# Kernel optimization log

Hardware: AMD Instinct MI355X
Metric: run time of the kernel (lower is better)

The kernel has to match this reference:

```python
import jax, jax.numpy as jnp
import numpy as np

B, T, D = 128, 150, 100
NQ, NS, NU = 50000, 2000, 20000
QNB, SNB, UNB, Q2NB = 4, 10, 10, 5
HOPS, RANK_K = 3, 10
NEG = -1e9


def _linear(x, W, b):
    return x @ W.T + b


def _aggregate(hops, agg_W, agg_b, last_W, last_b):
    # triangular multi-hop mean-aggregate, mirrors sqgkt.aggregate (dropout in eval mode)
    hops = list(hops)
    n = len(hops) - 1
    for i in range(n):
        for j in range(n - i):
            s = jnp.mean(hops[j + 1], axis=-2) + hops[j]
            hops[j] = jax.nn.relu(_linear(s, agg_W[j], agg_b[j]))
    return jax.nn.relu(_linear(hops[0], last_W, last_b))


def forward_impl(floats, ints):
    (emb_q, emb_q2, emb_s, emb_u, emb_r, w1_q, w2_q, lin_W, lin_b,
     Wih, Whh, bih, bhh, agg_W, agg_b, last_W, last_b,
     qW, qb, kW, kb, wW, wb, h0, c0) = floats
    (user, question, response, mask, q_neighbors, s_neighbors,
     u_neighbors, q_neighbors_2, qs_skill_ids) = ints

    jpos = jnp.arange(T)
    # detached question embeddings over the full sequence (recap scoring uses .detach())
    eq_sg = jax.lax.stop_gradient(emb_q)[question]  # [B,T,D]
    xs = (user.T[:-1], question.T[:-1], response.T[:-1], (mask == 1).T[:-1],
          question.T[1:], jnp.moveaxis(eq_sg, 1, 0)[1:], jnp.arange(T - 1))

    def predict(qs_concat, hist, hmask):
        # bilinear scores between question/skill embs and history states,
        # attention weights from MLP_W(cat(MLP_query(q), MLP_key(s)))
        g = jnp.einsum('bqd,bsd->bqs', qs_concat, hist)
        sq = _linear(qs_concat, qW, qb) @ wW[0, :D]   # [B,nq]
        sk = _linear(hist, kW, kb) @ wW[0, D:]        # [B,ns]
        score = sq[:, :, None] + sk[:, None, :] + wb[0]
        score = jnp.where(hmask[:, None, :], score, NEG)
        alpha = jax.nn.softmax(score.reshape(B, -1), axis=1)
        return jax.nn.sigmoid(jnp.sum(alpha * g.reshape(B, -1), axis=1))

    def step(carry, x):
        h, c, hist_state = carry
        u_t, q_t, r_t, m_t, q_next, eqn_sg, t = x
        # ---- question/skill multi-hop gather + aggregate (mask selects rows) ----
        n1 = q_neighbors[q_t]              # [B,QNB] skill ids
        n2 = s_neighbors[n1]               # [B,QNB,SNB] question ids
        n3 = q_neighbors[n2]               # [B,QNB,SNB,QNB] skill ids
        agg1 = _aggregate([emb_q[q_t], emb_s[n1], emb_q[n2], emb_s[n3]],
                          agg_W, agg_b, last_W, last_b)
        e_q = jnp.where(m_t[:, None], agg1, emb_q[q_t])
        # ---- user/question multi-hop gather + aggregate ----
        m1 = u_neighbors[u_t]              # [B,UNB] question ids
        m2 = q_neighbors_2[m1]             # [B,UNB,Q2NB] user ids
        m3 = u_neighbors[m2]               # [B,UNB,Q2NB,UNB] question ids
        agg2 = _aggregate([emb_u[u_t], emb_q2[m1], emb_u[m2], emb_q2[m3]],
                          agg_W, agg_b, last_W, last_b)
        e_q2 = jnp.where(m_t[:, None], agg2, emb_q2[q_t])
        emb_hat = w1_q * e_q + w2_q * e_q2
        # ---- LSTM step (torch LSTMCell gate order i,f,g,o) ----
        x_in = jax.nn.relu(_linear(jnp.concatenate([emb_hat, emb_r[r_t]], axis=1), lin_W, lin_b))
        gates = x_in @ Wih.T + bih + h @ Whh.T + bhh
        ig, fg, gg, og = jnp.split(gates, 4, axis=1)
        c = jax.nn.sigmoid(fg) * c + jax.nn.sigmoid(ig) * jnp.tanh(gg)
        h = jax.nn.sigmoid(og) * jnp.tanh(c)
        # ---- next-question + its related skills (fixed QNB skills/question) ----
        qs_concat = jnp.concatenate([emb_q[q_next][:, None], emb_s[qs_skill_ids[q_next]]], axis=1)
        # ---- soft recap: top-k past states by detached emb similarity ----
        scores = jnp.where(jpos[None, :] < t,
                           jnp.einsum('bjd,bd->bj', eq_sg, eqn_sg), -jnp.inf)
        top_vals, top_idx = jax.lax.top_k(scores, RANK_K)
        valid = jnp.isfinite(top_vals)     # fewer than K valid when t<=K
        sel = jnp.where(valid[:, :, None],
                        jnp.take_along_axis(hist_state, top_idx[:, :, None], axis=1), 0.0)
        hist = jnp.concatenate([h[:, None], sel], axis=1)      # [B,K+1,D]
        hmask = jnp.concatenate([jnp.ones((B, 1), bool), valid], axis=1)
        y = predict(qs_concat, hist, hmask)
        # torch skips the state_history write at t==0 (continue), so keep zeros there
        hist_state = hist_state.at[:, t].set(jnp.where(t > 0, h, 0.0))
        return (h, c, hist_state), y

    _, ys = jax.lax.scan(step, (h0, c0, jnp.zeros((B, T, D), jnp.float32)), xs)
    return jnp.concatenate([jnp.full((B, 1), 0.5, jnp.float32), ys.T], axis=1)


def setup_inputs():
    ks = jax.random.split(jax.random.key(0), 40)
    g = lambda i, shape, s=0.05: jax.random.normal(ks[i], shape, dtype=jnp.float32) * s
    ri = lambda i, shape, hi: jax.random.randint(ks[i], shape, 0, hi, dtype=jnp.int32)
    xav = float(np.sqrt(6.0 / (B + D)))  # xavier_uniform_ on a [B,D] zeros tensor
    return {
        'emb_q': g(0, (NQ, D)), 'emb_q2': g(1, (NQ, D)),
        'emb_s': g(2, (NS, D)), 'emb_u': g(3, (NU, D)),
        'emb_r': g(4, (2, D)),
        'w1_q': jnp.float32(0.5), 'w2_q': jnp.float32(0.5),
        'lin_W': g(5, (2 * D, 2 * D)), 'lin_b': jnp.zeros((2 * D,), jnp.float32),
        'Wih': g(6, (4 * D, 2 * D)), 'Whh': g(7, (4 * D, D)),
        'bih': jnp.zeros((4 * D,), jnp.float32), 'bhh': jnp.zeros((4 * D,), jnp.float32),
        'agg_W': g(8, (HOPS, D, D)), 'agg_b': jnp.zeros((HOPS, D), jnp.float32),
        'last_W': g(9, (D, D)), 'last_b': jnp.zeros((D,), jnp.float32),
        'qW': g(10, (D, D)), 'qb': jnp.zeros((D,), jnp.float32),
        'kW': g(11, (D, D)), 'kb': jnp.zeros((D,), jnp.float32),
        'wW': g(12, (1, 2 * D)), 'wb': jnp.zeros((1,), jnp.float32),
        'h0': jax.random.uniform(ks[13], (B, D), jnp.float32, -xav, xav),
        'c0': jax.random.uniform(ks[14], (B, D), jnp.float32, -xav, xav),
        'user': ri(15, (B, T), NU), 'question': ri(16, (B, T), NQ),
        'response': ri(17, (B, T), 2), 'mask': ri(18, (B, T), 2),
        'q_neighbors': ri(19, (NQ, QNB), NS), 's_neighbors': ri(20, (NS, SNB), NQ),
        'u_neighbors': ri(21, (NU, UNB), NQ), 'q_neighbors_2': ri(22, (NQ, Q2NB), NU),
        'qs_skill_ids': ri(23, (NQ, QNB), NS),
    }


def reference(emb_q, emb_q2, emb_s, emb_u, emb_r, w1_q, w2_q, lin_W, lin_b, Wih, Whh, bih, bhh, agg_W, agg_b, last_W, last_b, qW, qb, kW, kb, wW, wb, h0, c0, user, question, response, mask, q_neighbors, s_neighbors, u_neighbors, q_neighbors_2, qs_skill_ids):
    floats = (emb_q, emb_q2, emb_s, emb_u, emb_r, w1_q, w2_q, lin_W, lin_b,
              Wih, Whh, bih, bhh, agg_W, agg_b, last_W, last_b,
              qW, qb, kW, kb, wW, wb, h0, c0)
    ints = (user, question, response, mask, q_neighbors, s_neighbors,
            u_neighbors, q_neighbors_2, qs_skill_ids)
    return forward_impl(floats, ints)
```

## Files before the change

### kernel.cpp

```cpp
#include <hip/hip_runtime.h>
#include <hip/hip_bf16.h>

#define BB 128
#define TT 150
#define TS 149
#define NITEM (TS*BB)

typedef __attribute__((ext_vector_type(8))) short bf16x8;
typedef __attribute__((ext_vector_type(4))) float f32x4;

__device__ __forceinline__ float bf(__hip_bfloat16 x) { return __bfloat162float(x); }
__device__ __forceinline__ __hip_bfloat16 tobf(float x) { return __float2bfloat16(x); }
__device__ __forceinline__ float sigm(float x) { return 1.f / (1.f + expf(-x)); }

__device__ __forceinline__ unsigned pk2(float a, float b) {
  unsigned ua = __float_as_uint(a), ub = __float_as_uint(b);
  ua += 0x7fffu + ((ua >> 16) & 1u);
  ub += 0x7fffu + ((ub >> 16) & 1u);
  return (ua >> 16) | (ub & 0xffff0000u);
}
__device__ __forceinline__ float blo(unsigned u) { return __uint_as_float(u << 16); }
__device__ __forceinline__ float bhi(unsigned u) { return __uint_as_float(u & 0xffff0000u); }

#define PREP_N 3267131
__global__ __launch_bounds__(256, 4) void k_prep(
    const float* __restrict__ agg_W, const float* __restrict__ last_W,
    const float* __restrict__ lin_W, const float* __restrict__ Wih,
    const float* __restrict__ emb_q, const float* __restrict__ emb_q2,
    const float* __restrict__ emb_s, const float* __restrict__ emb_u,
    const int* __restrict__ q_nb, const int* __restrict__ s_nb,
    const int* __restrict__ u_nb, const int* __restrict__ q_nb2,
    const float* __restrict__ Whh,
    const float* __restrict__ qW, const float* __restrict__ qb,
    const float* __restrict__ kW, const float* __restrict__ kb,
    const float* __restrict__ wW, const float* __restrict__ wb,
    __hip_bfloat16* __restrict__ Wb, uint2* __restrict__ W0g, uint2* __restrict__ WLg,
    __hip_bfloat16* __restrict__ linB, __hip_bfloat16* __restrict__ wihB,
    uint2* __restrict__ gQ, uint2* __restrict__ gU,
    uint2* __restrict__ gT1Q, uint2* __restrict__ gT1U,
    uint4* __restrict__ WhP, float* __restrict__ kvqv,
    uint2* __restrict__ W0c, uint2* __restrict__ WLc)
{
  for (int v = blockIdx.x*256 + threadIdx.x; v < PREP_N; v += gridDim.x*256) {
    if (v < 65536) {
      int m = v >> 14, r = v & 16383, c = r >> 7, k = r & 127;
      const float* src = (m==0) ? agg_W+20000 : (m==1) ? agg_W+10000 : (m==2) ? agg_W : last_W;
      Wb[v] = tobf((c < 100 && k < 100) ? src[c*100+k] : 0.f);
    } else if (v < 70536) {
      int j = v - 65536; int mtx = j / 2500; j %= 2500;
      int k4 = j / 100, c = j % 100;
      const float* src = mtx ? last_W : agg_W;
      float4 a = *(const float4*)&src[c*100 + k4*4];
      (mtx ? WLg : W0g)[j] = make_uint2(pk2(a.x,a.y), pk2(a.z,a.w));
    } else if (v < 117128) {
      int j = v - 70536;
      int c = j / 224, k = j % 224;
      linB[j] = tobf((c < 200 && k < 200) ? lin_W[c*200+k] : 0.f);
    } else if (v < 206728) {
      int j = v - 117128;
      int c = j / 224, k = j % 224;
      wihB[j] = tobf((k < 200) ? Wih[c*200+k] : 0.f);
    } else if (v < 1456728) {
      int j = v - 206728, q = j / 25, k4 = j % 25;
      float sx=0.f,sy=0.f,sz=0.f,sw=0.f;
#pragma unroll
      for (int i = 0; i < 4; i++) {
        float4 e = *(const float4*)&emb_s[q_nb[q*4+i]*100 + k4*4];
        sx+=e.x; sy+=e.y; sz+=e.z; sw+=e.w;
      }
      float4 a = *(const float4*)&emb_q[q*100 + k4*4];
      gQ[j] = make_uint2(pk2(0.25f*sx+a.x, 0.25f*sy+a.y), pk2(0.25f*sz+a.z, 0.25f*sw+a.w));
    } else if (v < 1956728) {
      int j = v - 1456728, u = j / 25, k4 = j % 25;
      float sx=0.f,sy=0.f,sz=0.f,sw=0.f;
      for (int k = 0; k < 10; k++) {
        float4 e = *(const float4*)&emb_q2[u_nb[u*10+k]*100 + k4*4];
        sx+=e.x; sy+=e.y; sz+=e.z; sw+=e.w;
      }
      float4 a = *(const float4*)&emb_u[u*100 + k4*4];
      gU[j] = make_uint2(pk2(0.1f*sx+a.x, 0.1f*sy+a.y), pk2(0.1f*sz+a.z, 0.1f*sw+a.w));
    } else if (v < 2006728) {
      int j = v - 1956728, s = j / 25, k4 = j % 25;
      float sx=0.f,sy=0.f,sz=0.f,sw=0.f;
      for (int jj = 0; jj < 10; jj++) {
        float4 e = *(const float4*)&emb_q[s_nb[s*10+jj]*100 + k4*4];
        sx+=e.x; sy+=e.y; sz+=e.z; sw+=e.w;
      }
      float4 a = *(const float4*)&emb_s[s*100 + k4*4];
      gT1Q[j] = make_uint2(pk2(0.1f*sx+a.x, 0.1f*sy+a.y), pk2(0.1f*sz+a.z, 0.1f*sw+a.w));
    } else if (v < 3256728) {
      int j = v - 2006728, q = j / 25, k4 = j % 25;
      float sx=0.f,sy=0.f,sz=0.f,sw=0.f;
#pragma unroll
      for (int p = 0; p < 5; p++) {
        float4 e = *(const float4*)&emb_u[q_nb2[q*5+p]*100 + k4*4];
        sx+=e.x; sy+=e.y; sz+=e.z; sw+=e.w;
      }
      float4 a = *(const float4*)&emb_q2[q*100 + k4*4];
      gT1U[j] = make_uint2(pk2(0.2f*sx+a.x, 0.2f*sy+a.y), pk2(0.2f*sz+a.z, 0.2f*sw+a.w));
    } else if (v < 3261928) {
      int j = v - 3256728; int row = j / 13, k8 = j % 13;
      float vv[8];
#pragma unroll
      for (int r = 0; r < 8; r++) { int k = k8*8 + r; vv[r] = (k < 100) ? Whh[row*100 + k] : 0.f; }
      WhP[j] = make_uint4(pk2(vv[0],vv[1]), pk2(vv[2],vv[3]), pk2(vv[4],vv[5]), pk2(vv[6],vv[7]));
    } else if (v < 3262131) {
      int idx = v - 3261928;
      float s = 0.f;
      if (idx < 100)      { for (int c = 0; c < 100; c++) s += kW[c*100+idx] * wW[100+c]; kvqv[idx] = s; }
      else if (idx < 200) { int t2 = idx-100; for (int c = 0; c < 100; c++) s += qW[c*100+t2] * wW[c]; kvqv[idx] = s; }
      else if (idx == 200){ for (int c = 0; c < 100; c++) s += kb[c] * wW[100+c]; kvqv[200] = s; }
      else if (idx == 201){ for (int c = 0; c < 100; c++) s += qb[c] * wW[c]; kvqv[201] = s; }
      else kvqv[202] = wb[0];
    } else {
      int j = v - 3262131; int mtx = j / 2500; j %= 2500;
      int c = j / 25, k4 = j % 25;
      const float* src = mtx ? last_W : agg_W;
      float4 a = *(const float4*)&src[c*100 + k4*4];
      (mtx ? WLc : W0c)[j] = make_uint2(pk2(a.x,a.y), pk2(a.z,a.w));
    }
  }
}

__global__ __launch_bounds__(512, 6) void k_embhat(
    const float* __restrict__ emb_q, const float* __restrict__ emb_q2,
    const float* __restrict__ w1_q, const float* __restrict__ w2_q,
    const float* __restrict__ agg_b, const float* __restrict__ last_b,
    const int* __restrict__ user, const int* __restrict__ question, const int* __restrict__ mask,
    const int* __restrict__ q_nb, const int* __restrict__ s_nb,
    const int* __restrict__ u_nb, const int* __restrict__ q_nb2,
    const __hip_bfloat16* __restrict__ Wb,
    const uint2* __restrict__ W0c, const uint2* __restrict__ WLc,
    const uint2* __restrict__ gQ, const uint2* __restrict__ gU,
    const uint2* __restrict__ gT1Q, const uint2* __restrict__ gT1U,
    __hip_bfloat16* __restrict__ embhat)
{
  __shared__ __align__(16) char Ab[114*256];
  __shared__ __hip_bfloat16 Cb[114*100];
  __shared__ int n2[40], m2[50], n1[4], m1[10];
  float* S = (float*)Ab;
  const int tid = threadIdx.x, wid = tid >> 6, lane = tid & 63;
  const int l15 = lane & 15, lg = lane >> 4;
  const int item = blockIdx.x;
  const int t = item / BB, b = item % BB;
  const int qt = question[b*TT + t];
  const float w1 = w1_q[0], w2 = w2_q[0];

  if (mask[b*TT + t] != 1) {
    if (tid < 50) {
      const float2 q = *(const float2*)&emb_q[qt*100 + tid*2];
      const float2 p = *(const float2*)&emb_q2[qt*100 + tid*2];
      ((unsigned*)embhat)[item*50 + tid] = pk2(w1*q.x + w2*p.x, w1*q.y + w2*p.y);
    }
    return;
  }
  const int ut = user[b*TT + t];

  bf16x8 w2f[4];
  if (wid < 7) {
#pragma unroll
    for (int kc = 0; kc < 4; kc++)
      w2f[kc] = *(const bf16x8*)(Wb + (wid*16 + l15)*128 + kc*32 + lg*8);
  }

  for (int v = tid; v < 1102; v += 512) {
    if (v < 40) { int n1a = q_nb[qt*4 + v/10]; n2[v] = s_nb[n1a*10 + v%10]; }
    else if (v < 90) { int e = v-40; int m1a = u_nb[ut*10 + e/5]; m2[e] = q_nb2[m1a*5 + e%5]; }
    else if (v < 94) { n1[v-90] = q_nb[qt*4 + (v-90)]; }
    else if (v < 104) { m1[v-94] = u_nb[ut*10 + (v-94)]; }
    else {
      int z = v - 104, row, k4;
      if (z < 798) { row = z/7; k4 = 25 + z%7; }
      else if (z < 948) { int e = z-798; row = 90 + e/25; k4 = e%25; }
      else { int e = z-948; row = 110 + e/25; k4 = e%25; }
      int ofs = (row*256 + k4*8) ^ ((row&7)<<4);
// ... 109 lines not shown
      }
      int col = nt*16 + l15, r0 = mt*16 + lg*4;
      if (col < 100) {
#pragma unroll
        for (int r = 0; r < 4; r++)
          if (r0 + r < 114) Cb[(r0+r)*100 + col] = tobf(acc[r]);
      }
    }
  }
  __syncthreads();
  if (tid < 50) {
    int side = tid / 25, k4 = tid % 25;
    float4 b1q = *(const float4*)&agg_b[100 + k4*4];
    float4 b0q = *(const float4*)&agg_b[k4*4];
    float s0=0.f,s1=0.f,s2=0.f,s3=0.f, r0,r1,r2,r3;
    float inv;
    if (side == 0) {
      for (int a = 0; a < 4; a++) { RELU4(a, b1q, r0,r1,r2,r3); s0+=r0;s1+=r1;s2+=r2;s3+=r3; }
      inv = 0.25f; RELU4(16, b0q, r0,r1,r2,r3);
    } else {
      for (int a = 4; a < 14; a++) { RELU4(a, b1q, r0,r1,r2,r3); s0+=r0;s1+=r1;s2+=r2;s3+=r3; }
      inv = 0.1f; RELU4(17, b0q, r0,r1,r2,r3);
    }
    *(float4*)&S[side*100 + k4*4] = make_float4(inv*s0+r0, inv*s1+r1, inv*s2+r2, inv*s3+r3);
  }
  __syncthreads();
  if (tid < 200) {
    int side = tid / 100, c = tid % 100;
    const float4* xq = (const float4*)&S[side*100];
    float a0=0.f, a1=0.f, a2=0.f, a3=0.f;
    for (int k4 = 0; k4 < 25; k4++) {
      uint2 w = W0c[c*25 + k4];
      float4 xv = xq[k4];
      a0 = fmaf(blo(w.x), xv.x, a0);
      a1 = fmaf(bhi(w.x), xv.y, a1);
      a2 = fmaf(blo(w.y), xv.z, a2);
      a3 = fmaf(bhi(w.y), xv.w, a3);
    }
    S[200 + side*100 + c] = fmaxf(agg_b[c] + (a0+a1)+(a2+a3), 0.f);
  }
  __syncthreads();
  if (tid < 100) {
    int c = tid;
    const float4* xq0 = (const float4*)&S[200];
    const float4* xq1 = (const float4*)&S[300];
    float a0=0.f,a1=0.f,a2=0.f,a3=0.f, b0v=0.f,b1v=0.f,b2v=0.f,b3v=0.f;
    for (int k4 = 0; k4 < 25; k4++) {
      uint2 w = WLc[c*25 + k4];
      float4 x0v = xq0[k4], x1v = xq1[k4];
      a0 = fmaf(blo(w.x), x0v.x, a0); a1 = fmaf(bhi(w.x), x0v.y, a1);
      a2 = fmaf(blo(w.y), x0v.z, a2); a3 = fmaf(bhi(w.y), x0v.w, a3);
      b0v = fmaf(blo(w.x), x1v.x, b0v); b1v = fmaf(bhi(w.x), x1v.y, b1v);
      b2v = fmaf(blo(w.y), x1v.z, b2v); b3v = fmaf(bhi(w.y), x1v.w, b3v);
    }
    float dq = fmaxf(last_b[c] + (a0+a1)+(a2+a3), 0.f);
    float du = fmaxf(last_b[c] + (b0v+b1v)+(b2v+b3v), 0.f);
    embhat[item*100 + c] = tobf(w1*dq + w2*du);
  }
#undef RELU4
}

__global__ __launch_bounds__(512, 2) void k_lin(
    const float* __restrict__ emb_r, const float* __restrict__ lin_b,
    const float* __restrict__ bih, const float* __restrict__ bhh,
    const int* __restrict__ response,
    const __hip_bfloat16* __restrict__ embhat,
    const __hip_bfloat16* __restrict__ linB, const __hip_bfloat16* __restrict__ wihB,
    __hip_bfloat16* __restrict__ xg)
{
  __shared__ __align__(16) char Xt[64*512];
  __shared__ __align__(16) char Yt[64*512];
  const int tid = threadIdx.x, wid = tid >> 6, lane = tid & 63;
  const int l15 = lane & 15, lg = lane >> 4;
  const int t = blockIdx.x >> 1, rb = (blockIdx.x & 1) << 6;
  for (int v = tid; v < 7936; v += 512) {
    if (v < 7168) {
      int b = v / 112, c2 = v % 112; int col = c2*2;
      unsigned val;
      if (col < 100) val = ((const unsigned*)embhat)[(size_t)(t*128 + rb + b)*50 + c2];
      else if (col < 200) {
        int rt = response[(rb + b)*TT + t];
        val = pk2(emb_r[rt*100 + col - 100], emb_r[rt*100 + col - 99]);
      } else val = 0u;
      *(unsigned*)(Xt + ((b*512 + col*2) ^ ((b&7)<<4))) = val;
    } else {
      int e = v - 7168; int b = e / 12; int col = 200 + (e % 12)*2;
      *(unsigned*)(Yt + ((b*512 + col*2) ^ ((b&7)<<4))) = 0u;
    }
  }
  __syncthreads();
  for (int tp = wid; tp < 52; tp += 8) {
    int mt = tp / 13, nt = tp % 13;
    int arow = mt*16 + l15;
    f32x4 acc = {0.f,0.f,0.f,0.f};
#pragma unroll
    for (int kc = 0; kc < 7; kc++) {
      bf16x8 av = *(const bf16x8*)(Xt + ((arow*512 + kc*64 + lg*16) ^ ((arow&7)<<4)));
      bf16x8 bv = *(const bf16x8*)(linB + (nt*16 + l15)*224 + kc*32 + lg*8);
      acc = __builtin_amdgcn_mfma_f32_16x16x32_bf16(av, bv, acc, 0, 0, 0);
    }
    int col = nt*16 + l15, r0 = mt*16 + lg*4;
    if (col < 200) {
      float lbv = lin_b[col];
#pragma unroll
      for (int r = 0; r < 4; r++) {
        int row = r0 + r;
        *(__hip_bfloat16*)(Yt + ((row*512 + col*2) ^ ((row&7)<<4))) = tobf(fmaxf(acc[r] + lbv, 0.f));
      }
    }
  }
  __syncthreads();
  for (int tp = wid; tp < 100; tp += 8) {
    int mt = tp / 25, nt = tp % 25;
    int arow = mt*16 + l15;
    f32x4 acc = {0.f,0.f,0.f,0.f};
#pragma unroll
    for (int kc = 0; kc < 7; kc++) {
      bf16x8 av = *(const bf16x8*)(Yt + ((arow*512 + kc*64 + lg*16) ^ ((arow&7)<<4)));
      bf16x8 bv = *(const bf16x8*)(wihB + (nt*16 + l15)*224 + kc*32 + lg*8);
      acc = __builtin_amdgcn_mfma_f32_16x16x32_bf16(av, bv, acc, 0, 0, 0);
    }
    int col = nt*16 + l15, r0 = mt*16 + lg*4;
    float bs = bih[col] + bhh[col];
#pragma unroll
    for (int r = 0; r < 4; r++)
      xg[(size_t)(t*128 + rb + r0 + r)*400 + col] = tobf(acc[r] + bs);
  }
}

__global__ __launch_bounds__(256, 2) void k_topk(
    const float* __restrict__ emb_q, const int* __restrict__ question,
    int* __restrict__ topidx)
{
  __shared__ __align__(16) float Qb[150*104];
  __shared__ int qid[150];
  __shared__ float tval[1490];
  __shared__ int tidxs[1490];
  const int b = blockIdx.x, tid = threadIdx.x;
  if (tid < 150) qid[tid] = question[b*TT + tid];
  __syncthreads();
  for (int i = tid; i < 15000; i += 256) { int r = i/100, c = i%100; Qb[r*104+c] = emb_q[qid[r]*100+c]; }
// ... 1 lines not shown
  if (tid < TS) {
    const int t = tid;
    float* v = &tval[t*10]; int* ix = &tidxs[t*10];
    for (int p = 0; p < 10; p++) { v[p] = -3.0e38f; ix[p] = 0; }
    const float4* qrow = (const float4*)&Qb[(t+1)*104];
    for (int j = 0; j < t; j++) {
      const float4* r = (const float4*)&Qb[j*104];
      float s = 0.f;
#pragma unroll
      for (int k4 = 0; k4 < 25; k4++) {
        float4 a = qrow[k4], c = r[k4];
        s += a.x*c.x + a.y*c.y + a.z*c.z + a.w*c.w;
      }
      if (s > v[9]) {
        int p = 9;
        while (p > 0 && s > v[p-1]) { v[p] = v[p-1]; ix[p] = ix[p-1]; p--; }
        v[p] = s; ix[p] = j;
      }
    }
    for (int p = 0; p < 10; p++) topidx[(t*BB + b)*10 + p] = ix[p];
  }
}

__global__ __launch_bounds__(448, 1) void k_lstm(
    const uint4* __restrict__ WhP,
    const __hip_bfloat16* __restrict__ xg,
    const float* __restrict__ h0, const float* __restrict__ c0,
    unsigned* __restrict__ hstG, float* __restrict__ out)
{
  __shared__ unsigned hbfu[52];
  __shared__ float gates[400];
  const int b = blockIdx.x, tid = threadIdx.x;
  uint4 w[13];
  if (tid < 400) {
#pragma unroll
    for (int k8 = 0; k8 < 13; k8++) w[k8] = WhP[tid*13 + k8];
  }
  float c = 0.f;
  if (tid < 100) c = c0[b*100 + tid];
  if (tid < 50) hbfu[tid] = pk2(h0[b*100 + 2*tid], h0[b*100 + 2*tid + 1]);
  else if (tid < 52) hbfu[tid] = 0u;
  if (tid == 128) out[b*TT] = 0.5f;
  float xpre = 0.f;
  if (tid < 400) xpre = bf(xg[(size_t)b*400 + tid]);
  __syncthreads();
  for (int t = 0; t < TS; t++) {
    if (tid < 400) {
      float a0 = xpre, a1 = 0.f, a2 = 0.f, a3 = 0.f;
      if (t + 1 < TS) xpre = bf(xg[((size_t)(t+1)*BB + b)*400 + tid]);
#pragma unroll
      for (int k8 = 0; k8 < 13; k8++) {
        uint4 h = *(const uint4*)&hbfu[k8*4];
        a0 = fmaf(blo(w[k8].x), blo(h.x), a0);
        a1 = fmaf(bhi(w[k8].x), bhi(h.x), a1);
        a2 = fmaf(blo(w[k8].y), blo(h.y), a2);
        a3 = fmaf(bhi(w[k8].y), bhi(h.y), a3);
        a0 = fmaf(blo(w[k8].z), blo(h.z), a0);
        a1 = fmaf(bhi(w[k8].z), bhi(h.z), a1);
        a2 = fmaf(blo(w[k8].w), blo(h.w), a2);
        a3 = fmaf(bhi(w[k8].w), bhi(h.w), a3);
      }
      gates[tid] = (a0 + a1) + (a2 + a3);
    }
    __syncthreads();
    if (tid < 100) {
      float cc = sigm(gates[100+tid])*c + sigm(gates[tid])*tanhf(gates[200+tid]);
      c = cc;
      float hn = sigm(gates[300+tid])*tanhf(cc);
      float hp = __shfl_xor(hn, 1);
      if (!(tid & 1)) {
        unsigned pkv = pk2(hn, hp);
        hbfu[tid >> 1] = pkv;
        hstG[((size_t)b*TS + t)*50 + (tid >> 1)] = pkv;
      }
    }
    __syncthreads();
  }
}

__global__ __launch_bounds__(512, 1) void k_attn(
    const float* __restrict__ emb_q, const float* __restrict__ emb_s,
    const int* __restrict__ question, const int* __restrict__ qs_skill,
    const int* __restrict__ topidx, const unsigned* __restrict__ hstG,
    const float* __restrict__ kvqv, float* __restrict__ out)
{
  __shared__ __align__(16) uint2 Hl[149*26];
  __shared__ __align__(16) float qsb[8][500];
  __shared__ float sqb[8][5];
  __shared__ float skt[152];
  __shared__ __align__(16) float qvl[100];
  const int b = blockIdx.x, tid = threadIdx.x;
  const int wv = tid >> 6, lane = tid & 63;
  for (int i = tid; i < 149*25; i += 512) {
    int r = i / 25, cc = i % 25;
    Hl[r*26 + cc] = *(const uint2*)&hstG[((size_t)b*TS + r)*50 + cc*2];
  }
  if (tid < 100) qvl[tid] = kvqv[100 + tid];
  __syncthreads();
  const float ck = kvqv[200], cq = kvqv[201], wb0 = kvqv[202];
  if (tid < 298) {
    int r = tid >> 1, half = tid & 1;
    float s0=0.f,s1=0.f,s2=0.f,s3=0.f;
    for (int cc = half*13; cc < (half ? 25 : 13); cc++) {
      uint2 u = Hl[r*26 + cc];
      float4 kvv = *(const float4*)&kvqv[cc*4];
      s0 = fmaf(blo(u.x), kvv.x, s0); s1 = fmaf(bhi(u.x), kvv.y, s1);
      s2 = fmaf(blo(u.y), kvv.z, s2); s3 = fmaf(bhi(u.y), kvv.w, s3);
    }
    float s = (s0+s1)+(s2+s3);
    s += __shfl_xor(s, 1);
    if (!half) skt[r] = s + ck;
  }
  __syncthreads();
  for (int t0 = 0; t0 < TS; t0 += 8) {
    int t = t0 + wv;
    if (t >= TS) continue;
    const int qn = question[b*TT + t + 1];
    for (int e = lane; e < 500; e += 64) {
      int q = e / 100;
      qsb[wv][e] = (q == 0) ? emb_q[qn*100 + e]
                            : emb_s[qs_skill[qn*4 + q - 1]*100 + e%100];
    }
    if (lane >= 55 && lane < 60) {
      int q = lane - 55;
      const float4* qq = (const float4*)&qsb[wv][q*100];
      float s0=0.f,s1=0.f,s2=0.f,s3=0.f;
      for (int cc = 0; cc < 25; cc++) {
        float4 a = qq[cc]; float4 qv4 = *(const float4*)&qvl[cc*4];
        s0 = fmaf(a.x, qv4.x, s0); s1 = fmaf(a.y, qv4.y, s1);
        s2 = fmaf(a.z, qv4.z, s2); s3 = fmaf(a.w, qv4.w, s3);
      }
      sqb[wv][q] = (s0+s1)+(s2+s3) + cq;
    }
    float scv = -3.0e38f, gval = 0.f;
    if (lane < 55) {
      int q = lane / 11, s = lane % 11;
      int j; bool valid = true;
      float sk = 0.f;
      if (s == 0) { j = t; sk = skt[t]; }
      else {
        int cnt = t < 10 ? t : 10;
        if (s - 1 < cnt) {
          j = topidx[((size_t)t*BB + b)*10 + s - 1];
          sk = (j == 0) ? ck : skt[j];
        } else { j = -1; valid = false; }
      }
      if ((valid && j > 0) || (s == 0 && j == 0)) {
        const uint2* hr = &Hl[(j > 0 ? j : 0)*26];
        const float4* qq = (const float4*)&qsb[wv][q*100];
        float g0=0.f,g1=0.f,g2=0.f,g3=0.f;
        for (int cc = 0; cc < 25; cc++) {
          uint2 u = hr[cc]; float4 a = qq[cc];
          g0 = fmaf(blo(u.x), a.x, g0); g1 = fmaf(bhi(u.x), a.y, g1);
          g2 = fmaf(blo(u.y), a.z, g2); g3 = fmaf(bhi(u.y), a.w, g3);
        }
        gval = (g0+g1)+(g2+g3);
      }
      scv = valid ? (sqb[wv][q] + sk + wb0) : -1e9f;
    }
    float m = scv;
#pragma unroll
    for (int o = 32; o; o >>= 1) m = fmaxf(m, __shfl_xor(m, o));
    float ex = (lane < 55) ? expf(scv - m) : 0.f;
    float num = ex * gval, den = ex;
#pragma unroll
    for (int o = 32; o; o >>= 1) { num += __shfl_xor(num, o); den += __shfl_xor(den, o); }
    if (lane == 0) out[b*TT + t + 1] = sigm(num/den);
  }
}

extern "C" void kernel_launch(void* const* d_in, const int* in_sizes, int n_in,
                              void* d_out, int out_size, void* d_ws, size_t ws_size,
                              hipStream_t stream) {
  const float* emb_q  = (const float*)d_in[0];
  const float* emb_q2 = (const float*)d_in[1];
  const float* emb_s  = (const float*)d_in[2];
  const float* emb_u  = (const float*)d_in[3];
// ... 9 lines not shown
  const float* agg_W  = (const float*)d_in[13];
  const float* agg_b  = (const float*)d_in[14];
  const float* last_W = (const float*)d_in[15];
  const float* last_b = (const float*)d_in[16];
  const float* qW     = (const float*)d_in[17];
  const float* qb     = (const float*)d_in[18];
  const float* kW     = (const float*)d_in[19];
  const float* kb     = (const float*)d_in[20];
  const float* wW     = (const float*)d_in[21];
  const float* wb     = (const float*)d_in[22];
  const float* h0     = (const float*)d_in[23];
  const float* c0     = (const float*)d_in[24];
  const int* user      = (const int*)d_in[25];
  const int* question  = (const int*)d_in[26];
  const int* response  = (const int*)d_in[27];
  const int* mask      = (const int*)d_in[28];
  const int* q_nb      = (const int*)d_in[29];
  const int* s_nb      = (const int*)d_in[30];
  const int* u_nb      = (const int*)d_in[31];
  const int* q_nb2     = (const int*)d_in[32];
  const int* qs_skill  = (const int*)d_in[33];

  char* ws = (char*)d_ws;
  __hip_bfloat16* embhat = (__hip_bfloat16*)(ws + 0);
  __hip_bfloat16* xg     = (__hip_bfloat16*)(ws + 3814400);
  int*            topidx = (int*)(ws + 19072000);
  __hip_bfloat16* Wb     = (__hip_bfloat16*)(ws + 19834880);
  uint2*          W0g    = (uint2*)(ws + 19965952);
  uint2*          WLg    = (uint2*)(ws + 19985952);
  __hip_bfloat16* linB   = (__hip_bfloat16*)(ws + 20005952);
  __hip_bfloat16* wihB   = (__hip_bfloat16*)(ws + 20099136);
  uint2*          gQ     = (uint2*)(ws + 20278336);
  uint2*          gU     = (uint2*)(ws + 30278336);
  uint2*          gT1Q   = (uint2*)(ws + 34278336);
  uint2*          gT1U   = (uint2*)(ws + 34678336);
  uint4*          WhP    = (uint4*)(ws + 44678336);
  float*          kvqv   = (float*)(ws + 44761536);
  unsigned*       hstG   = (unsigned*)(ws + 44762560);
  uint2*          W0c    = (uint2*)(ws + 48576960);
  uint2*          WLc    = (uint2*)(ws + 48596960);

  k_prep<<<2048, 256, 0, stream>>>(agg_W, last_W, lin_W, Wih,
                                   emb_q, emb_q2, emb_s, emb_u,
                                   q_nb, s_nb, u_nb, q_nb2,
                                   Whh, qW, qb, kW, kb, wW, wb,
                                   Wb, W0g, WLg, linB, wihB, gQ, gU, gT1Q, gT1U,
                                   WhP, kvqv, W0c, WLc);
  k_embhat<<<NITEM, 512, 0, stream>>>(emb_q, emb_q2, w1_q, w2_q,
                                      agg_b, last_b,
                                      user, question, mask, q_nb, s_nb, u_nb, q_nb2,
                                      Wb, W0c, WLc, gQ, gU, gT1Q, gT1U, embhat);
  k_lin<<<TS*2, 512, 0, stream>>>(emb_r, lin_b, bih, bhh, response, embhat,
                                  linB, wihB, xg);
  k_topk<<<128, 256, 0, stream>>>(emb_q, question, topidx);
  k_lstm<<<128, 448, 0, stream>>>(WhP, xg, h0, c0, hstG, (float*)d_out);
  k_attn<<<128, 512, 0, stream>>>(emb_q, emb_s, question, qs_skill,
                                  topidx, hstG, kvqv, (float*)d_out);
}
```

Baseline: 902.9 us.

## Move final aggregate layers into batched MFMA chain kernel and fuse LSTM with attention

```diff
diff --git a/kernel.cpp b/kernel.cpp
--- a/kernel.cpp
+++ b/kernel.cpp
@@ -22,7 +22,7 @@
 __device__ __forceinline__ float blo(unsigned u) { return __uint_as_float(u << 16); }
 __device__ __forceinline__ float bhi(unsigned u) { return __uint_as_float(u & 0xffff0000u); }
 
-#define PREP_N 3267131
+#define PREP_N 3251931
 __global__ __launch_bounds__(256, 4) void k_prep(
     const float* __restrict__ agg_W, const float* __restrict__ last_W,
     const float* __restrict__ lin_W, const float* __restrict__ Wih,
@@ -30,38 +30,30 @@
     const float* __restrict__ emb_s, const float* __restrict__ emb_u,
     const int* __restrict__ q_nb, const int* __restrict__ s_nb,
     const int* __restrict__ u_nb, const int* __restrict__ q_nb2,
-    const float* __restrict__ Whh,
     const float* __restrict__ qW, const float* __restrict__ qb,
     const float* __restrict__ kW, const float* __restrict__ kb,
     const float* __restrict__ wW, const float* __restrict__ wb,
-    __hip_bfloat16* __restrict__ Wb, uint2* __restrict__ W0g, uint2* __restrict__ WLg,
+    __hip_bfloat16* __restrict__ Wb,
     __hip_bfloat16* __restrict__ linB, __hip_bfloat16* __restrict__ wihB,
     uint2* __restrict__ gQ, uint2* __restrict__ gU,
     uint2* __restrict__ gT1Q, uint2* __restrict__ gT1U,
-    uint4* __restrict__ WhP, float* __restrict__ kvqv,
-    uint2* __restrict__ W0c, uint2* __restrict__ WLc)
+    float* __restrict__ kvqv)
 {
   for (int v = blockIdx.x*256 + threadIdx.x; v < PREP_N; v += gridDim.x*256) {
     if (v < 65536) {
       int m = v >> 14, r = v & 16383, c = r >> 7, k = r & 127;
       const float* src = (m==0) ? agg_W+20000 : (m==1) ? agg_W+10000 : (m==2) ? agg_W : last_W;
       Wb[v] = tobf((c < 100 && k < 100) ? src[c*100+k] : 0.f);
-    } else if (v < 70536) {
-      int j = v - 65536; int mtx = j / 2500; j %= 2500;
-      int k4 = j / 100, c = j % 100;
-      const float* src = mtx ? last_W : agg_W;
-      float4 a = *(const float4*)&src[c*100 + k4*4];
-      (mtx ? WLg : W0g)[j] = make_uint2(pk2(a.x,a.y), pk2(a.z,a.w));
-    } else if (v < 117128) {
-      int j = v - 70536;
+    } else if (v < 112128) {
+      int j = v - 65536;
       int c = j / 224, k = j % 224;
       linB[j] = tobf((c < 200 && k < 200) ? lin_W[c*200+k] : 0.f);
-    } else if (v < 206728) {
-      int j = v - 117128;
+    } else if (v < 201728) {
+      int j = v - 112128;
       int c = j / 224, k = j % 224;
       wihB[j] = tobf((k < 200) ? Wih[c*200+k] : 0.f);
-    } else if (v < 1456728) {
-      int j = v - 206728, q = j / 25, k4 = j % 25;
+    } else if (v < 1451728) {
+      int j = v - 201728, q = j / 25, k4 = j % 25;
       float sx=0.f,sy=0.f,sz=0.f,sw=0.f;
 #pragma unroll
       for (int i = 0; i < 4; i++) {
@@ -70,8 +62,8 @@
       }
       float4 a = *(const float4*)&emb_q[q*100 + k4*4];
       gQ[j] = make_uint2(pk2(0.25f*sx+a.x, 0.25f*sy+a.y), pk2(0.25f*sz+a.z, 0.25f*sw+a.w));
-    } else if (v < 1956728) {
-      int j = v - 1456728, u = j / 25, k4 = j % 25;
+    } else if (v < 1951728) {
+      int j = v - 1451728, u = j / 25, k4 = j % 25;
       float sx=0.f,sy=0.f,sz=0.f,sw=0.f;
       for (int k = 0; k < 10; k++) {
         float4 e = *(const float4*)&emb_q2[u_nb[u*10+k]*100 + k4*4];
@@ -79,8 +71,8 @@
       }
       float4 a = *(const float4*)&emb_u[u*100 + k4*4];
       gU[j] = make_uint2(pk2(0.1f*sx+a.x, 0.1f*sy+a.y), pk2(0.1f*sz+a.z, 0.1f*sw+a.w));
-    } else if (v < 2006728) {
-      int j = v - 1956728, s = j / 25, k4 = j % 25;
+    } else if (v < 2001728) {
+      int j = v - 1951728, s = j / 25, k4 = j % 25;
       float sx=0.f,sy=0.f,sz=0.f,sw=0.f;
       for (int jj = 0; jj < 10; jj++) {
         float4 e = *(const float4*)&emb_q[s_nb[s*10+jj]*100 + k4*4];
@@ -88,8 +80,8 @@
       }
       float4 a = *(const float4*)&emb_s[s*100 + k4*4];
       gT1Q[j] = make_uint2(pk2(0.1f*sx+a.x, 0.1f*sy+a.y), pk2(0.1f*sz+a.z, 0.1f*sw+a.w));
-    } else if (v < 3256728) {
-      int j = v - 2006728, q = j / 25, k4 = j % 25;
+    } else if (v < 3251728) {
+      int j = v - 2001728, q = j / 25, k4 = j % 25;
       float sx=0.f,sy=0.f,sz=0.f,sw=0.f;
 #pragma unroll
       for (int p = 0; p < 5; p++) {
@@ -98,26 +90,14 @@
       }
       float4 a = *(const float4*)&emb_q2[q*100 + k4*4];
       gT1U[j] = make_uint2(pk2(0.2f*sx+a.x, 0.2f*sy+a.y), pk2(0.2f*sz+a.z, 0.2f*sw+a.w));
-    } else if (v < 3261928) {
-      int j = v - 3256728; int row = j / 13, k8 = j % 13;
-      float vv[8];
-#pragma unroll
-      for (int r = 0; r < 8; r++) { int k = k8*8 + r; vv[r] = (k < 100) ? Whh[row*100 + k] : 0.f; }
-      WhP[j] = make_uint4(pk2(vv[0],vv[1]), pk2(vv[2],vv[3]), pk2(vv[4],vv[5]), pk2(vv[6],vv[7]));
-    } else if (v < 3262131) {
-      int idx = v - 3261928;
+    } else {
+      int idx = v - 3251728;
       float s = 0.f;
       if (idx < 100)      { for (int c = 0; c < 100; c++) s += kW[c*100+idx] * wW[100+c]; kvqv[idx] = s; }
       else if (idx < 200) { int t2 = idx-100; for (int c = 0; c < 100; c++) s += qW[c*100+t2] * wW[c]; kvqv[idx] = s; }
       else if (idx == 200){ for (int c = 0; c < 100; c++) s += kb[c] * wW[100+c]; kvqv[200] = s; }
       else if (idx == 201){ for (int c = 0; c < 100; c++) s += qb[c] * wW[c]; kvqv[201] = s; }
       else kvqv[202] = wb[0];
-    } else {
-      int j = v - 3262131; int mtx = j / 2500; j %= 2500;
-      int c = j / 25, k4 = j % 25;
-      const float* src = mtx ? last_W : agg_W;
-      float4 a = *(const float4*)&src[c*100 + k4*4];
-      (mtx ? WLc : W0c)[j] = make_uint2(pk2(a.x,a.y), pk2(a.z,a.w));
     }
   }
 }
@@ -125,20 +105,18 @@
 __global__ __launch_bounds__(512, 6) void k_embhat(
     const float* __restrict__ emb_q, const float* __restrict__ emb_q2,
     const float* __restrict__ w1_q, const float* __restrict__ w2_q,
-    const float* __restrict__ agg_b, const float* __restrict__ last_b,
+    const float* __restrict__ agg_b,
     const int* __restrict__ user, const int* __restrict__ question, const int* __restrict__ mask,
     const int* __restrict__ q_nb, const int* __restrict__ s_nb,
     const int* __restrict__ u_nb, const int* __restrict__ q_nb2,
     const __hip_bfloat16* __restrict__ Wb,
-    const uint2* __restrict__ W0c, const uint2* __restrict__ WLc,
     const uint2* __restrict__ gQ, const uint2* __restrict__ gU,
     const uint2* __restrict__ gT1Q, const uint2* __restrict__ gT1U,
-    __hip_bfloat16* __restrict__ embhat)
+    unsigned* __restrict__ u0)
 {
   __shared__ __align__(16) char Ab[114*256];
   __shared__ __hip_bfloat16 Cb[114*100];
   __shared__ int n2[40], m2[50], n1[4], m1[10];
-  float* S = (float*)Ab;
   const int tid = threadIdx.x, wid = tid >> 6, lane = tid & 63;
   const int l15 = lane & 15, lg = lane >> 4;
   const int item = blockIdx.x;
@@ -150,7 +128,7 @@
     if (tid < 50) {
       const float2 q = *(const float2*)&emb_q[qt*100 + tid*2];
       const float2 p = *(const float2*)&emb_q2[qt*100 + tid*2];
-      ((unsigned*)embhat)[item*50 + tid] = pk2(w1*q.x + w2*p.x, w1*q.y + w2*p.y);
+      u0[(size_t)item*100 + tid] = pk2(w1*q.x + w2*p.x, w1*q.y + w2*p.y);
     }
     return;
   }
@@ -306,80 +284,119 @@
       for (int a = 4; a < 14; a++) { RELU4(a, b1q, r0,r1,r2,r3); s0+=r0;s1+=r1;s2+=r2;s3+=r3; }
       inv = 0.1f; RELU4(17, b0q, r0,r1,r2,r3);
     }
-    *(float4*)&S[side*100 + k4*4] = make_float4(inv*s0+r0, inv*s1+r1, inv*s2+r2, inv*s3+r3);
-  }
-  __syncthreads();
-  if (tid < 200) {
-    int side = tid / 100, c = tid % 100;
-    const float4* xq = (const float4*)&S[side*100];
-    float a0=0.f, a1=0.f, a2=0.f, a3=0.f;
-    for (int k4 = 0; k4 < 25; k4++) {
-      uint2 w = W0c[c*25 + k4];
-      float4 xv = xq[k4];
-      a0 = fmaf(blo(w.x), xv.x, a0);
-      a1 = fmaf(bhi(w.x), xv.y, a1);
-      a2 = fmaf(blo(w.y), xv.z, a2);
-      a3 = fmaf(bhi(w.y), xv.w, a3);
-    }
-    S[200 + side*100 + c] = fmaxf(agg_b[c] + (a0+a1)+(a2+a3), 0.f);
-  }
-  __syncthreads();
-  if (tid < 100) {
-    int c = tid;
-    const float4* xq0 = (const float4*)&S[200];
-    const float4* xq1 = (const float4*)&S[300];
-    float a0=0.f,a1=0.f,a2=0.f,a3=0.f, b0v=0.f,b1v=0.f,b2v=0.f,b3v=0.f;
-    for (int k4 = 0; k4 < 25; k4++) {
-      uint2 w = WLc[c*25 + k4];
-      float4 x0v = xq0[k4], x1v = xq1[k4];
-      a0 = fmaf(blo(w.x), x0v.x, a0); a1 = fmaf(bhi(w.x), x0v.y, a1);
-      a2 = fmaf(blo(w.y), x0v.z, a2); a3 = fmaf(bhi(w.y), x0v.w, a3);
-      b0v = fmaf(blo(w.x), x1v.x, b0v); b1v = fmaf(bhi(w.x), x1v.y, b1v);
-      b2v = fmaf(blo(w.y), x1v.z, b2v); b3v = fmaf(bhi(w.y), x1v.w, b3v);
-    }
-    float dq = fmaxf(last_b[c] + (a0+a1)+(a2+a3), 0.f);
-    float du = fmaxf(last_b[c] + (b0v+b1v)+(b2v+b3v), 0.f);
-    embhat[item*100 + c] = tobf(w1*dq + w2*du);
+    float x0 = inv*s0+r0, x1 = inv*s1+r1, x2 = inv*s2+r2, x3 = inv*s3+r3;
+    *(uint2*)&u0[(size_t)item*100 + side*50 + k4*2] = make_uint2(pk2(x0,x1), pk2(x2,x3));
   }
 #undef RELU4
 }
 
-__global__ __launch_bounds__(512, 2) void k_lin(
-    const float* __restrict__ emb_r, const float* __restrict__ lin_b,
-    const float* __restrict__ bih, const float* __restrict__ bhh,
-    const int* __restrict__ response,
-    const __hip_bfloat16* __restrict__ embhat,
+__global__ __launch_bounds__(512, 4) void k_chain(
+    const float* __restrict__ emb_r,
+    const float* __restrict__ agg_b, const float* __restrict__ last_b,
+    const float* __restrict__ lin_b, const float* __restrict__ bih,
+    const float* __restrict__ bhh,
+    const float* __restrict__ w1_q, const float* __restrict__ w2_q,
+    const int* __restrict__ response, const int* __restrict__ mask,
+    const unsigned* __restrict__ u0,
+    const __hip_bfloat16* __restrict__ Wb,
     const __hip_bfloat16* __restrict__ linB, const __hip_bfloat16* __restrict__ wihB,
     __hip_bfloat16* __restrict__ xg)
 {
-  __shared__ __align__(16) char Xt[64*512];
-  __shared__ __align__(16) char Yt[64*512];
+  __shared__ __align__(16) char B1[64*256];
+  __shared__ __align__(16) char B2[64*256];
+  __shared__ int msk[32];
   const int tid = threadIdx.x, wid = tid >> 6, lane = tid & 63;
   const int l15 = lane & 15, lg = lane >> 4;
-  const int t = blockIdx.x >> 1, rb = (blockIdx.x & 1) << 6;
-  for (int v = tid; v < 7936; v += 512) {
-    if (v < 7168) {
-      int b = v / 112, c2 = v % 112; int col = c2*2;
-      unsigned val;
-      if (col < 100) val = ((const unsigned*)embhat)[(size_t)(t*128 + rb + b)*50 + c2];
-      else if (col < 200) {
-        int rt = response[(rb + b)*TT + t];
-        val = pk2(emb_r[rt*100 + col - 100], emb_r[rt*100 + col - 99]);
-      } else val = 0u;
-      *(unsigned*)(Xt + ((b*512 + col*2) ^ ((b&7)<<4))) = val;
+  const int t = blockIdx.x >> 2, rb = (blockIdx.x & 3) << 5;
+  const float w1 = w1_q[0], w2 = w2_q[0];
+  for (int v = tid; v < 2528; v += 512) {
+    if (v < 1600) {
+      int row = v / 25, k4 = v % 25;
+      int item = t*128 + rb + (row >> 1), side = row & 1;
+      uint2 val = *(const uint2*)&u0[(size_t)item*100 + side*50 + k4*2];
+      *(uint2*)(B1 + ((row*256 + k4*8) ^ ((row&7)<<4))) = val;
+    } else if (v < 2048) {
+      int e = v-1600; int row = e/7, k4 = 25 + e%7;
+      *(uint2*)(B1 + ((row*256 + k4*8) ^ ((row&7)<<4))) = make_uint2(0u,0u);
+    } else if (v < 2496) {
+      int e = v-2048; int row = e/7, k4 = 25 + e%7;
+      *(uint2*)(B2 + ((row*256 + k4*8) ^ ((row&7)<<4))) = make_uint2(0u,0u);
     } else {
-      int e = v - 7168; int b = e / 12; int col = 200 + (e % 12)*2;
-      *(unsigned*)(Yt + ((b*512 + col*2) ^ ((b&7)<<4))) = 0u;
-    }
-  }
-  __syncthreads();
-  for (int tp = wid; tp < 52; tp += 8) {
+      int i = v - 2496;
+      msk[i] = mask[(rb+i)*TT + t];
+    }
+  }
+  __syncthreads();
+  for (int tp = wid; tp < 28; tp += 8) {
+    int mt = tp / 7, nt = tp % 7;
+    int arow = mt*16 + l15;
+    f32x4 acc = {0.f,0.f,0.f,0.f};
+#pragma unroll
+    for (int kc = 0; kc < 4; kc++) {
+      bf16x8 av = *(const bf16x8*)(B1 + ((arow*256 + kc*64 + lg*16) ^ ((arow&7)<<4)));
+      bf16x8 bv = *(const bf16x8*)(Wb + 32768 + (nt*16 + l15)*128 + kc*32 + lg*8);
+      acc = __builtin_amdgcn_mfma_f32_16x16x32_bf16(av, bv, acc, 0, 0, 0);
+    }
+    int col = nt*16 + l15, r0 = mt*16 + lg*4;
+    if (col < 100) {
+      float b0v = agg_b[col];
+#pragma unroll
+      for (int r = 0; r < 4; r++) {
+        int row = r0 + r;
+        *(__hip_bfloat16*)(B2 + ((row*256 + col*2) ^ ((row&7)<<4))) = tobf(fmaxf(acc[r] + b0v, 0.f));
+      }
+    }
+  }
+  __syncthreads();
+  for (int tp = wid; tp < 28; tp += 8) {
+    int mt = tp / 7, nt = tp % 7;
+    int arow = mt*16 + l15;
+    f32x4 acc = {0.f,0.f,0.f,0.f};
+#pragma unroll
+    for (int kc = 0; kc < 4; kc++) {
+      bf16x8 av = *(const bf16x8*)(B2 + ((arow*256 + kc*64 + lg*16) ^ ((arow&7)<<4)));
+      bf16x8 bv = *(const bf16x8*)(Wb + 49152 + (nt*16 + l15)*128 + kc*32 + lg*8);
+      acc = __builtin_amdgcn_mfma_f32_16x16x32_bf16(av, bv, acc, 0, 0, 0);
+    }
+    int col = nt*16 + l15, r0 = mt*16 + lg*4;
+    if (col < 100) {
+      float blv = last_b[col];
+#pragma unroll
+      for (int pp = 0; pp < 2; pp++) {
+        int il = (r0 >> 1) + pp;
+        int item = t*128 + rb + il;
+        float e;
+        if (msk[il] == 1)
+          e = w1*fmaxf(acc[2*pp] + blv, 0.f) + w2*fmaxf(acc[2*pp+1] + blv, 0.f);
+        else
+          e = bf(((const __hip_bfloat16*)u0)[(size_t)item*200 + col]);
+        *(__hip_bfloat16*)(B1 + ((il*512 + col*2) ^ ((il&7)<<4))) = tobf(e);
+      }
+    }
+  }
+  for (int v = tid; v < 1984; v += 512) {
+    if (v < 1600) {
+      int row = v / 50, c2 = v % 50; int col = 100 + c2*2;
+      int rt = response[(rb+row)*TT + t];
+      unsigned val = pk2(emb_r[rt*100 + c2*2], emb_r[rt*100 + c2*2 + 1]);
+      *(unsigned*)(B1 + ((row*512 + col*2) ^ ((row&7)<<4))) = val;
+    } else {
+      int e = v - 1600; int row = e/12, col = 200 + (e%12)*2;
+      *(unsigned*)(B1 + ((row*512 + col*2) ^ ((row&7)<<4))) = 0u;
+    }
+  }
+  __syncthreads();
+  for (int v = tid; v < 384; v += 512) {
+    int row = v/12, col = 200 + (v%12)*2;
+    *(unsigned*)(B2 + ((row*512 + col*2) ^ ((row&7)<<4))) = 0u;
+  }
+  for (int tp = wid; tp < 26; tp += 8) {
     int mt = tp / 13, nt = tp % 13;
     int arow = mt*16 + l15;
     f32x4 acc = {0.f,0.f,0.f,0.f};
 #pragma unroll
     for (int kc = 0; kc < 7; kc++) {
-      bf16x8 av = *(const bf16x8*)(Xt + ((arow*512 + kc*64 + lg*16) ^ ((arow&7)<<4)));
+      bf16x8 av = *(const bf16x8*)(B1 + ((arow*512 + kc*64 + lg*16) ^ ((arow&7)<<4)));
       bf16x8 bv = *(const bf16x8*)(linB + (nt*16 + l15)*224 + kc*32 + lg*8);
       acc = __builtin_amdgcn_mfma_f32_16x16x32_bf16(av, bv, acc, 0, 0, 0);
     }
@@ -389,18 +406,18 @@
 #pragma unroll
       for (int r = 0; r < 4; r++) {
         int row = r0 + r;
-        *(__hip_bfloat16*)(Yt + ((row*512 + col*2) ^ ((row&7)<<4))) = tobf(fmaxf(acc[r] + lbv, 0.f));
-      }
-    }
-  }
-  __syncthreads();
-  for (int tp = wid; tp < 100; tp += 8) {
+        *(__hip_bfloat16*)(B2 + ((row*512 + col*2) ^ ((row&7)<<4))) = tobf(fmaxf(acc[r] + lbv, 0.f));
+      }
+    }
+  }
+  __syncthreads();
+  for (int tp = wid; tp < 50; tp += 8) {
     int mt = tp / 25, nt = tp % 25;
     int arow = mt*16 + l15;
     f32x4 acc = {0.f,0.f,0.f,0.f};
 #pragma unroll
     for (int kc = 0; kc < 7; kc++) {
-      bf16x8 av = *(const bf16x8*)(Yt + ((arow*512 + kc*64 + lg*16) ^ ((arow&7)<<4)));
+      bf16x8 av = *(const bf16x8*)(B2 + ((arow*512 + kc*64 + lg*16) ^ ((arow&7)<<4)));
       bf16x8 bv = *(const bf16x8*)(wihB + (nt*16 + l15)*224 + kc*32 + lg*8);
       acc = __builtin_amdgcn_mfma_f32_16x16x32_bf16(av, bv, acc, 0, 0, 0);
     }
@@ -448,90 +465,68 @@
   }
 }
 
-__global__ __launch_bounds__(448, 1) void k_lstm(
-    const uint4* __restrict__ WhP,
-    const __hip_bfloat16* __restrict__ xg,
+__global__ __launch_bounds__(512, 1) void k_seq(
+    const float* __restrict__ Whh, const __hip_bfloat16* __restrict__ xg,
     const float* __restrict__ h0, const float* __restrict__ c0,
-    unsigned* __restrict__ hstG, float* __restrict__ out)
-{
-  __shared__ unsigned hbfu[52];
-  __shared__ float gates[400];
-  const int b = blockIdx.x, tid = threadIdx.x;
-  uint4 w[13];
-  if (tid < 400) {
-#pragma unroll
-    for (int k8 = 0; k8 < 13; k8++) w[k8] = WhP[tid*13 + k8];
-  }
-  float c = 0.f;
-  if (tid < 100) c = c0[b*100 + tid];
-  if (tid < 50) hbfu[tid] = pk2(h0[b*100 + 2*tid], h0[b*100 + 2*tid + 1]);
-  else if (tid < 52) hbfu[tid] = 0u;
-  if (tid == 128) out[b*TT] = 0.5f;
-  float xpre = 0.f;
-  if (tid < 400) xpre = bf(xg[(size_t)b*400 + tid]);
-  __syncthreads();
-  for (int t = 0; t < TS; t++) {
-    if (tid < 400) {
-      float a0 = xpre, a1 = 0.f, a2 = 0.f, a3 = 0.f;
-      if (t + 1 < TS) xpre = bf(xg[((size_t)(t+1)*BB + b)*400 + tid]);
-#pragma unroll
-      for (int k8 = 0; k8 < 13; k8++) {
-        uint4 h = *(const uint4*)&hbfu[k8*4];
-        a0 = fmaf(blo(w[k8].x), blo(h.x), a0);
-        a1 = fmaf(bhi(w[k8].x), bhi(h.x), a1);
-        a2 = fmaf(blo(w[k8].y), blo(h.y), a2);
-        a3 = fmaf(bhi(w[k8].y), bhi(h.y), a3);
-        a0 = fmaf(blo(w[k8].z), blo(h.z), a0);
-        a1 = fmaf(bhi(w[k8].z), bhi(h.z), a1);
-        a2 = fmaf(blo(w[k8].w), blo(h.w), a2);
-        a3 = fmaf(bhi(w[k8].w), bhi(h.w), a3);
-      }
-      gates[tid] = (a0 + a1) + (a2 + a3);
-    }
-    __syncthreads();
-    if (tid < 100) {
-      float cc = sigm(gates[100+tid])*c + sigm(gates[tid])*tanhf(gates[200+tid]);
-      c = cc;
-      float hn = sigm(gates[300+tid])*tanhf(cc);
-      float hp = __shfl_xor(hn, 1);
-      if (!(tid & 1)) {
-        unsigned pkv = pk2(hn, hp);
-        hbfu[tid >> 1] = pkv;
-        hstG[((size_t)b*TS + t)*50 + (tid >> 1)] = pkv;
-      }
-    }
-    __syncthreads();
-  }
-}
-
-__global__ __launch_bounds__(512, 1) void k_attn(
     const float* __restrict__ emb_q, const float* __restrict__ emb_s,
     const int* __restrict__ question, const int* __restrict__ qs_skill,
-    const int* __restrict__ topidx, const unsigned* __restrict__ hstG,
-    const float* __restrict__ kvqv, float* __restrict__ out)
+    const int* __restrict__ topidx, const float* __restrict__ kvqv,
+    float* __restrict__ out)
 {
-  __shared__ __align__(16) uint2 Hl[149*26];
+  __shared__ __align__(16) float hist[TS*100];
+  __shared__ __align__(16) float h_l[100];
+  __shared__ float gates[400];
   __shared__ __align__(16) float qsb[8][500];
   __shared__ float sqb[8][5];
   __shared__ float skt[152];
   __shared__ __align__(16) float qvl[100];
   const int b = blockIdx.x, tid = threadIdx.x;
   const int wv = tid >> 6, lane = tid & 63;
-  for (int i = tid; i < 149*25; i += 512) {
-    int r = i / 25, cc = i % 25;
-    Hl[r*26 + cc] = *(const uint2*)&hstG[((size_t)b*TS + r)*50 + cc*2];
-  }
-  if (tid < 100) qvl[tid] = kvqv[100 + tid];
-  __syncthreads();
+  float4 w[25];
+  if (tid < 400) {
+#pragma unroll
+    for (int k4 = 0; k4 < 25; k4++) w[k4] = *(const float4*)&Whh[tid*100 + k4*4];
+  }
+  float c = 0.f;
+  if (tid < 100) { c = c0[b*100 + tid]; h_l[tid] = h0[b*100 + tid]; }
+  if (tid >= 128 && tid < 228) qvl[tid-128] = kvqv[100 + (tid-128)];
+  if (tid == 480) out[b*TT] = 0.5f;
+  float xpre = 0.f;
+  if (tid < 400) xpre = bf(xg[(size_t)b*400 + tid]);
+  __syncthreads();
+  for (int t = 0; t < TS; t++) {
+    if (tid < 400) {
+      float a0 = xpre, a1 = 0.f, a2 = 0.f, a3 = 0.f;
+      if (t + 1 < TS) xpre = bf(xg[((size_t)(t+1)*BB + b)*400 + tid]);
+#pragma unroll
+      for (int k4 = 0; k4 < 25; k4++) {
+        float4 h4 = *(const float4*)&h_l[k4*4];
+        a0 = fmaf(w[k4].x, h4.x, a0);
+        a1 = fmaf(w[k4].y, h4.y, a1);
+        a2 = fmaf(w[k4].z, h4.z, a2);
+        a3 = fmaf(w[k4].w, h4.w, a3);
+      }
+      gates[tid] = (a0 + a1) + (a2 + a3);
+    }
+    __syncthreads();
+    if (tid < 100) {
+      float cc = sigm(gates[100+tid])*c + sigm(gates[tid])*tanhf(gates[200+tid]);
+      c = cc;
+      float hn = sigm(gates[300+tid])*tanhf(cc);
+      h_l[tid] = hn;
+      hist[t*100 + tid] = hn;
+    }
+    __syncthreads();
+  }
   const float ck = kvqv[200], cq = kvqv[201], wb0 = kvqv[202];
   if (tid < 298) {
     int r = tid >> 1, half = tid & 1;
     float s0=0.f,s1=0.f,s2=0.f,s3=0.f;
-    for (int cc = half*13; cc < (half ? 25 : 13); cc++) {
-      uint2 u = Hl[r*26 + cc];
-      float4 kvv = *(const float4*)&kvqv[cc*4];
-      s0 = fmaf(blo(u.x), kvv.x, s0); s1 = fmaf(bhi(u.x), kvv.y, s1);
-      s2 = fmaf(blo(u.y), kvv.z, s2); s3 = fmaf(bhi(u.y), kvv.w, s3);
+    for (int k4 = half*13; k4 < (half ? 25 : 13); k4++) {
+      float4 h4 = *(const float4*)&hist[r*100 + k4*4];
+      float4 kv4 = *(const float4*)&kvqv[k4*4];
+      s0 = fmaf(h4.x, kv4.x, s0); s1 = fmaf(h4.y, kv4.y, s1);
+      s2 = fmaf(h4.z, kv4.z, s2); s3 = fmaf(h4.w, kv4.w, s3);
     }
     float s = (s0+s1)+(s2+s3);
     s += __shfl_xor(s, 1);
@@ -551,8 +546,8 @@
       int q = lane - 55;
       const float4* qq = (const float4*)&qsb[wv][q*100];
       float s0=0.f,s1=0.f,s2=0.f,s3=0.f;
-      for (int cc = 0; cc < 25; cc++) {
-        float4 a = qq[cc]; float4 qv4 = *(const float4*)&qvl[cc*4];
+      for (int k4 = 0; k4 < 25; k4++) {
+        float4 a = qq[k4]; float4 qv4 = *(const float4*)&qvl[k4*4];
         s0 = fmaf(a.x, qv4.x, s0); s1 = fmaf(a.y, qv4.y, s1);
         s2 = fmaf(a.z, qv4.z, s2); s3 = fmaf(a.w, qv4.w, s3);
       }
@@ -571,14 +566,15 @@
           sk = (j == 0) ? ck : skt[j];
         } else { j = -1; valid = false; }
       }
-      if ((valid && j > 0) || (s == 0 && j == 0)) {
-        const uint2* hr = &Hl[(j > 0 ? j : 0)*26];
+      if ((s == 0) || (valid && j > 0)) {
+        int row = (s == 0) ? t : j;
+        const float4* hr = (const float4*)&hist[row*100];
         const float4* qq = (const float4*)&qsb[wv][q*100];
         float g0=0.f,g1=0.f,g2=0.f,g3=0.f;
-        for (int cc = 0; cc < 25; cc++) {
-          uint2 u = hr[cc]; float4 a = qq[cc];
-          g0 = fmaf(blo(u.x), a.x, g0); g1 = fmaf(bhi(u.x), a.y, g1);
-          g2 = fmaf(blo(u.y), a.z, g2); g3 = fmaf(bhi(u.y), a.w, g3);
+        for (int k4 = 0; k4 < 25; k4++) {
+          float4 h4 = hr[k4]; float4 a = qq[k4];
+          g0 = fmaf(h4.x, a.x, g0); g1 = fmaf(h4.y, a.y, g1);
+          g2 = fmaf(h4.z, a.z, g2); g3 = fmaf(h4.w, a.w, g3);
         }
         gval = (g0+g1)+(g2+g3);
       }
@@ -634,38 +630,30 @@
   const int* qs_skill  = (const int*)d_in[33];
 
   char* ws = (char*)d_ws;
-  __hip_bfloat16* embhat = (__hip_bfloat16*)(ws + 0);
-  __hip_bfloat16* xg     = (__hip_bfloat16*)(ws + 3814400);
-  int*            topidx = (int*)(ws + 19072000);
-  __hip_bfloat16* Wb     = (__hip_bfloat16*)(ws + 19834880);
-  uint2*          W0g    = (uint2*)(ws + 19965952);
-  uint2*          WLg    = (uint2*)(ws + 19985952);
-  __hip_bfloat16* linB   = (__hip_bfloat16*)(ws + 20005952);
-  __hip_bfloat16* wihB   = (__hip_bfloat16*)(ws + 20099136);
-  uint2*          gQ     = (uint2*)(ws + 20278336);
-  uint2*          gU     = (uint2*)(ws + 30278336);
-  uint2*          gT1Q   = (uint2*)(ws + 34278336);
-  uint2*          gT1U   = (uint2*)(ws + 34678336);
-  uint4*          WhP    = (uint4*)(ws + 44678336);
-  float*          kvqv   = (float*)(ws + 44761536);
-  unsigned*       hstG   = (unsigned*)(ws + 44762560);
-  uint2*          W0c    = (uint2*)(ws + 48576960);
-  uint2*          WLc    = (uint2*)(ws + 48596960);
+  unsigned*       u0     = (unsigned*)(ws + 0);
+  __hip_bfloat16* xg     = (__hip_bfloat16*)(ws + 7628800);
+  int*            topidx = (int*)(ws + 22886400);
+  __hip_bfloat16* Wb     = (__hip_bfloat16*)(ws + 23649280);
+  __hip_bfloat16* linB   = (__hip_bfloat16*)(ws + 23780352);
+  __hip_bfloat16* wihB   = (__hip_bfloat16*)(ws + 23873536);
+  uint2*          gQ     = (uint2*)(ws + 24052736);
+  uint2*          gU     = (uint2*)(ws + 34052736);
+  uint2*          gT1Q   = (uint2*)(ws + 38052736);
+  uint2*          gT1U   = (uint2*)(ws + 38452736);
+  float*          kvqv   = (float*)(ws + 48452736);
 
   k_prep<<<2048, 256, 0, stream>>>(agg_W, last_W, lin_W, Wih,
                                    emb_q, emb_q2, emb_s, emb_u,
                                    q_nb, s_nb, u_nb, q_nb2,
-                                   Whh, qW, qb, kW, kb, wW, wb,
-                                   Wb, W0g, WLg, linB, wihB, gQ, gU, gT1Q, gT1U,
-                                   WhP, kvqv, W0c, WLc);
-  k_embhat<<<NITEM, 512, 0, stream>>>(emb_q, emb_q2, w1_q, w2_q,
-                                      agg_b, last_b,
+                                   qW, qb, kW, kb, wW, wb,
+                                   Wb, linB, wihB, gQ, gU, gT1Q, gT1U, kvqv);
+  k_embhat<<<NITEM, 512, 0, stream>>>(emb_q, emb_q2, w1_q, w2_q, agg_b,
                                       user, question, mask, q_nb, s_nb, u_nb, q_nb2,
-                                      Wb, W0c, WLc, gQ, gU, gT1Q, gT1U, embhat);
-  k_lin<<<TS*2, 512, 0, stream>>>(emb_r, lin_b, bih, bhh, response, embhat,
-                                  linB, wihB, xg);
+                                      Wb, gQ, gU, gT1Q, gT1U, u0);
+  k_chain<<<TS*4, 512, 0, stream>>>(emb_r, agg_b, last_b, lin_b, bih, bhh,
+                                    w1_q, w2_q, response, mask, u0,
+                                    Wb, linB, wihB, xg);
   k_topk<<<128, 256, 0, stream>>>(emb_q, question, topidx);
-  k_lstm<<<128, 448, 0, stream>>>(WhP, xg, h0, c0, hstG, (float*)d_out);
-  k_attn<<<128, 512, 0, stream>>>(emb_q, emb_s, question, qs_skill,
-                                  topidx, hstG, kvqv, (float*)d_out);
+  k_seq<<<128, 512, 0, stream>>>(Whh, xg, h0, c0, emb_q, emb_s,
+                                 question, qs_skill, topidx, kvqv, (float*)d_out);
 }
```

Measured after the change: 834.3 us. -7.6%, faster.
